# Kernel tuning notes

Measured on AMD Instinct MI355X. Metric: run time of the kernel, lower is better.

The kernel has to match this reference:

```python
import jax, jax.numpy as jnp
import numpy as np

N, E = 50000, 800000
F_IN, C_PRE, C, G_HID = 16, 32, 64, 64
EPS = 1e-5


def graph_norm(x, batch, w, b, ms):
    # PyG GraphNorm over a single graph (batch all zeros)
    cnt = jax.ops.segment_sum(jnp.ones((x.shape[0], 1), x.dtype), batch, num_segments=1)
    mean = jax.ops.segment_sum(x, batch, num_segments=1) / cnt
    out = x - mean[batch] * ms
    var = jax.ops.segment_sum(out * out, batch, num_segments=1) / cnt
    std = jnp.sqrt(var + EPS)
    return w * out / std[batch] + b


def ggnn_conv(h, edge_index, edge_attr,
              gw1, gb1, gw2, gb2, gw3, gb3,
              zw, zb, rw, rb, hw, hb):
    n = h.shape[0]
    loops = jnp.arange(n)
    row = jnp.concatenate([edge_index[0], loops])  # sources (x_j)
    col = jnp.concatenate([edge_index[1], loops])  # targets (x_i), aggregation index
    ea = jnp.concatenate([edge_attr, jnp.ones((n, 1), h.dtype)], axis=0)
    deg = jax.ops.segment_sum(jnp.ones(col.shape[0], h.dtype), col, num_segments=n)
    dis = jnp.where(deg > 0, deg ** -0.5, 0.0)
    norm = dis[row] * dis[col]
    x_j = h[row]
    x_i = h[col]
    g = jnp.concatenate([x_i, x_j, ea], axis=-1)            # [E+N, 2C+1]
    g = jax.nn.relu(g @ gw1 + gb1)
    g = jax.nn.relu(g @ gw2 + gb2)
    gate = jax.nn.sigmoid(g @ gw3 + gb3)                     # [E+N, 1]
    msg = gate * (norm[:, None] * x_j)
    aggr = jax.ops.segment_sum(msg, col, num_segments=n)     # scatter-add
    zi = jnp.concatenate([h, aggr], axis=-1)
    z = jax.nn.sigmoid(zi @ zw + zb)
    r = jax.nn.sigmoid(zi @ rw + rb)
    hc = jax.nn.relu(jnp.concatenate([r * h, aggr], axis=-1) @ hw + hb)
    return (1.0 - z) * h + z * hc


def setup_inputs() -> dict:
    key = jax.random.key(0)
    ks = iter(jax.random.split(key, 40))

    def lin(k, fi, fo):
        return jax.random.normal(k, (fi, fo), jnp.float32) / np.sqrt(fi)

    inp = {
        'x': jax.random.normal(next(ks), (N, F_IN), jnp.float32),
        'edge_index': jax.random.randint(next(ks), (2, E), 0, N),
        'edge_attr': jax.random.uniform(next(ks), (E, 1), jnp.float32),
        'batch': jnp.zeros((N,), jnp.int32),
        'preproc_w': lin(next(ks), F_IN, C_PRE), 'preproc_b': jnp.zeros((C_PRE,), jnp.float32),
        'gn_pre_w': jnp.ones((C_PRE,), jnp.float32), 'gn_pre_b': jnp.zeros((C_PRE,), jnp.float32), 'gn_pre_ms': jnp.ones((C_PRE,), jnp.float32),
        'init_w': lin(next(ks), C_PRE, C), 'init_b': jnp.zeros((C,), jnp.float32),
        'gn_init_w': jnp.ones((C,), jnp.float32), 'gn_init_b': jnp.zeros((C,), jnp.float32), 'gn_init_ms': jnp.ones((C,), jnp.float32),
        'gate_w1': lin(next(ks), 2 * C + 1, G_HID), 'gate_b1': jnp.zeros((G_HID,), jnp.float32),
        'gate_w2': lin(next(ks), G_HID, G_HID), 'gate_b2': jnp.zeros((G_HID,), jnp.float32),
        'gate_w3': lin(next(ks), G_HID, 1), 'gate_b3': jnp.zeros((1,), jnp.float32),
        'lin_z_w': lin(next(ks), 2 * C, C), 'lin_z_b': jnp.zeros((C,), jnp.float32),
        'lin_r_w': lin(next(ks), 2 * C, C), 'lin_r_b': jnp.zeros((C,), jnp.float32),
        'lin_h_w': lin(next(ks), 2 * C, C), 'lin_h_b': jnp.zeros((C,), jnp.float32),
        'gn_ggnn_w': jnp.ones((C,), jnp.float32), 'gn_ggnn_b': jnp.zeros((C,), jnp.float32), 'gn_ggnn_ms': jnp.ones((C,), jnp.float32),
        'fc1_w': lin(next(ks), 2 * C, C), 'fc1_b': jnp.zeros((C,), jnp.float32),
        'gn_fc1_w': jnp.ones((C,), jnp.float32), 'gn_fc1_b': jnp.zeros((C,), jnp.float32), 'gn_fc1_ms': jnp.ones((C,), jnp.float32),
        'fc2_w': lin(next(ks), C, 2), 'fc2_b': jnp.zeros((2,), jnp.float32),
    }
    return inp


def reference(x, edge_index, edge_attr, batch,
              preproc_w, preproc_b, gn_pre_w, gn_pre_b, gn_pre_ms,
              init_w, init_b, gn_init_w, gn_init_b, gn_init_ms,
              gate_w1, gate_b1, gate_w2, gate_b2, gate_w3, gate_b3,
              lin_z_w, lin_z_b, lin_r_w, lin_r_b, lin_h_w, lin_h_b,
              gn_ggnn_w, gn_ggnn_b, gn_ggnn_ms,
              fc1_w, fc1_b, gn_fc1_w, gn_fc1_b, gn_fc1_ms,
              fc2_w, fc2_b):
    n_layers = 4
    h = x @ preproc_w + preproc_b
    h = graph_norm(h, batch, gn_pre_w, gn_pre_b, gn_pre_ms)
    h = jax.nn.relu(h)
    h0 = h @ init_w + init_b
    h0 = graph_norm(h0, batch, gn_init_w, gn_init_b, gn_init_ms)
    h0 = jax.nn.relu(h0)
    h = h0
    for _ in range(n_layers):  # tied GGNN layer
        h = ggnn_conv(h, edge_index, edge_attr,
                      gate_w1, gate_b1, gate_w2, gate_b2, gate_w3, gate_b3,
                      lin_z_w, lin_z_b, lin_r_w, lin_r_b, lin_h_w, lin_h_b)
        h = graph_norm(h, batch, gn_ggnn_w, gn_ggnn_b, gn_ggnn_ms)
    out = jnp.concatenate([h0, h], axis=1)
    out = out @ fc1_w + fc1_b
    out = graph_norm(out, batch, gn_fc1_w, gn_fc1_b, gn_fc1_ms)
    out = jax.nn.relu(out)
    out = out @ fc2_w + fc2_b  # [N, 2] logits
    return out
```

## Files before the change

### kernel.cpp

```cpp
#include <hip/hip_runtime.h>

#define GN_EPS 1e-5f

typedef _Float16 half8 __attribute__((ext_vector_type(8)));
typedef float floatx4 __attribute__((ext_vector_type(4)));

__device__ __forceinline__ float sigmoidf_(float x){ return 1.0f/(1.0f+__expf(-x)); }
__device__ __forceinline__ float bcast_(float v, int k){
  return __int_as_float(__builtin_amdgcn_readlane(__float_as_int(v), k));
}

__global__ void cnt_init_kernel(int* cnt, int n){
  int i = blockIdx.x*blockDim.x+threadIdx.x;
  if (i < n) cnt[i] = 1;
}
__global__ void cnt_kernel(const int* __restrict__ ei, int* cnt, int E){
  int e = blockIdx.x*blockDim.x+threadIdx.x;
  if (e < E) atomicAdd(&cnt[ei[E+e]], 1);
}
__global__ void dis_from_cnt_kernel(const int* __restrict__ cnt, float* dis, int n){
  int i = blockIdx.x*blockDim.x+threadIdx.x;
  if (i < n) dis[i] = rsqrtf((float)cnt[i]);
}
__global__ __launch_bounds__(256) void scan1_kernel(const int* __restrict__ cnt,
                                                    int* loc, int* bsum, int n){
  __shared__ int s[256];
  int t = threadIdx.x, i = blockIdx.x*256 + t;
  int v = (i < n) ? cnt[i] : 0;
  s[t] = v; __syncthreads();
  #pragma unroll
  for (int d = 1; d < 256; d <<= 1){
    int u = (t >= d) ? s[t-d] : 0; __syncthreads();
    s[t] += u; __syncthreads();
  }
  if (i < n) loc[i] = s[t] - v;
  if (t == 255) bsum[blockIdx.x] = s[255];
}
__global__ __launch_bounds__(256) void scan2_kernel(int* bsum, int nb){
  __shared__ int s[256];
  int t = threadIdx.x;
  int v = (t < nb) ? bsum[t] : 0;
  s[t] = v; __syncthreads();
  #pragma unroll
  for (int d = 1; d < 256; d <<= 1){
    int u = (t >= d) ? s[t-d] : 0; __syncthreads();
    s[t] += u; __syncthreads();
  }
  if (t < nb) bsum[t] = s[t] - v;
}
__global__ void scan3_kernel(const int* __restrict__ loc, const int* __restrict__ bsum,
                             int* rowptr, int n, int total){
  int i = blockIdx.x*blockDim.x+threadIdx.x;
  if (i < n) rowptr[i] = loc[i] + bsum[i >> 8];
  if (i == 0) rowptr[n] = total;
}
__global__ void scatter_kernel(const int* __restrict__ ei, const float* __restrict__ ea,
                               const int* __restrict__ rowptr, int* fill,
                               unsigned* sd, _Float16* ea2, int E, int n){
  int idx = blockIdx.x*blockDim.x+threadIdx.x;
  int tot = E + n;
  if (idx >= tot) return;
  int r, c; float v;
  if (idx < E){ r = ei[idx]; c = ei[E+idx]; v = ea[idx]; }
  else        { r = c = idx - E; v = 1.0f; }
  int j = rowptr[c] + atomicAdd(&fill[c], 1);
  sd[j] = (unsigned)r | ((unsigned)c << 16);
  ea2[j] = (_Float16)v;
}

__global__ __launch_bounds__(256) void wprep_kernel(
    const float* __restrict__ w1, const float* __restrict__ zw,
    const float* __restrict__ rw, const float* __restrict__ hw,
    const float* __restrict__ fw, const float* __restrict__ w2,
    _Float16* __restrict__ wp){
  int idx = blockIdx.x*256 + threadIdx.x;
  if (idx < 8192){
    int t=idx>>10, kh=(idx>>9)&1, g=(idx>>7)&3, l=(idx>>3)&15, j=idx&7;
    int kg=(t>=4?64:0)+kh*32+g*8+j;
    wp[idx] = (_Float16)w1[kg*64 + (t&3)*16 + l];
  } else if (idx < 40960){
    int m=(idx-8192)>>13, k=(idx-8192)&8191;
    int t=(k>>11)&3, kh=(k>>9)&3, g=(k>>7)&3, l=(k>>3)&15, j=k&7;
    const float* W = (m==0)?zw:((m==1)?rw:((m==2)?hw:fw));
    wp[idx] = (_Float16)W[(kh*32+g*8+j)*64 + t*16 + l];
  } else if (idx < 45056){
    int k = idx-40960;
    int t=(k>>10)&3, kh=(k>>9)&1, g=(k>>7)&3, l=(k>>3)&15, j=k&7;
    wp[idx] = (_Float16)w2[(kh*32+g*8+j)*64 + t*16 + l];
  }
}

template<int K_IN, int C_OUT>
__global__ __launch_bounds__(256) void mm1_kernel(
    const float* __restrict__ x, const float* __restrict__ W,
    const float* __restrict__ b, float* __restrict__ y, int n){
  __shared__ float sW[K_IN*C_OUT];
  for (int i = threadIdx.x; i < K_IN*C_OUT; i += 256) sW[i] = W[i];
  __syncthreads();
  const int lane = threadIdx.x & 63;
  const int col  = (lane < C_OUT) ? lane : 0;
  const float bias = b[col];
  int wid = (blockIdx.x*256 + threadIdx.x) >> 6;
  int nw  = (gridDim.x*256) >> 6;
  for (int i = wid; i < n; i += nw){
    float xv = (lane < K_IN) ? x[(size_t)i*K_IN + lane] : 0.0f;
    float a0 = bias, a1 = 0.0f;
    #pragma unroll
    for (int k = 0; k < K_IN; k += 2){
      a0 += bcast_(xv, k  ) * sW[(k  )*C_OUT + col];
      a1 += bcast_(xv, k+1) * sW[(k+1)*C_OUT + col];
    }
    if (lane < C_OUT) y[(size_t)i*C_OUT + lane] = a0 + a1;
  }
}

template<int RELU, int WRITE_H0>
__global__ __launch_bounds__(256) void normpq_kernel(
    const float* __restrict__ hin, float* __restrict__ hout,
    float* __restrict__ h0out,
    const float* __restrict__ stats,
    const float* __restrict__ gw, const float* __restrict__ gb,
    const float* __restrict__ gms,
    const _Float16* __restrict__ w1p, const float* __restrict__ b1,
    _Float16* __restrict__ Ph, _Float16* __restrict__ QH, int n)
{
  __shared__ _Float16 sB[8192];
  __shared__ float sSO[128];
  for (int i = threadIdx.x; i < 1024; i += 256)
    ((half8*)sB)[i] = ((const half8*)w1p)[i];
  if (threadIdx.x < 64){
    int ch = threadIdx.x;
    float invN = 1.0f/(float)n;
    float mean = stats[ch]*invN;
    float mm = mean*gms[ch];
    float var = stats[64+ch]*invN - mm*(2.0f*mean - mm);
    float inv = rsqrtf(fmaxf(var,0.f)+GN_EPS);
    float sc = inv*gw[ch];
    sSO[ch] = sc;
    sSO[64+ch] = gb[ch] - mm*sc;
  }
  __syncthreads();
  const int lane = threadIdx.x & 63;
  const int g16 = lane>>4, l16 = lane&15;
  float scA[8], ofA[8], scB[8], ofB[8];
  #pragma unroll
  for (int j = 0; j < 8; ++j){
    scA[j]=sSO[g16*8+j];    ofA[j]=sSO[64+g16*8+j];
    scB[j]=sSO[32+g16*8+j]; ofB[j]=sSO[96+g16*8+j];
  }
  float b1f[4];
  #pragma unroll
  for (int t = 0; t < 4; ++t) b1f[t] = b1[t*16 + l16];

  int wid = (blockIdx.x*blockDim.x + threadIdx.x) >> 6;
  int nw  = (gridDim.x*blockDim.x) >> 6;
  int tiles = (n + 15) >> 4;
  for (int tile = wid; tile < tiles; tile += nw){
    int base = tile*16;
    int na = min(base + l16, n-1);
    const float* hp = hin + (size_t)na*64;
    float4 a0 = *(const float4*)(hp + g16*8);
    float4 a1 = *(const float4*)(hp + g16*8 + 4);
    float4 c0 = *(const float4*)(hp + 32 + g16*8);
    float4 c1 = *(const float4*)(hp + 32 + g16*8 + 4);
    float va[8] = {a0.x,a0.y,a0.z,a0.w,a1.x,a1.y,a1.z,a1.w};
    float vb[8] = {c0.x,c0.y,c0.z,c0.w,c1.x,c1.y,c1.z,c1.w};
    half8 af0, af1;
    #pragma unroll
    for (int j = 0; j < 8; ++j){
      float v = va[j]*scA[j] + ofA[j];
      if (RELU) v = fmaxf(v, 0.f);
      va[j] = v; af0[j] = (_Float16)v;
      float u = vb[j]*scB[j] + ofB[j];
      if (RELU) u = fmaxf(u, 0.f);
      vb[j] = u; af1[j] = (_Float16)u;
    }
    float* op = hout + (size_t)na*64;
    *(float4*)(op + g16*8)       = (float4){va[0],va[1],va[2],va[3]};
    *(float4*)(op + g16*8 + 4)   = (float4){va[4],va[5],va[6],va[7]};
    *(float4*)(op + 32 + g16*8)  = (float4){vb[0],vb[1],vb[2],vb[3]};
    *(float4*)(op + 32 + g16*8+4)= (float4){vb[4],vb[5],vb[6],vb[7]};
    if (WRITE_H0){
      float* o2 = h0out + (size_t)na*64;
      *(float4*)(o2 + g16*8)       = (float4){va[0],va[1],va[2],va[3]};
      *(float4*)(o2 + g16*8 + 4)   = (float4){va[4],va[5],va[6],va[7]};
      *(float4*)(o2 + 32 + g16*8)  = (float4){vb[0],vb[1],vb[2],vb[3]};
      *(float4*)(o2 + 32 + g16*8+4)= (float4){vb[4],vb[5],vb[6],vb[7]};
    }
    *(half8*)(QH + (size_t)na*128 + 64 + g16*8) = af0;
    *(half8*)(QH + (size_t)na*128 + 96 + g16*8) = af1;

    floatx4 acc[8];
    #pragma unroll
    for (int t = 0; t < 8; ++t){
      float bv = (t < 4) ? b1f[t] : 0.0f;
      acc[t] = (floatx4){bv, bv, bv, bv};
    }
    #pragma unroll
    for (int t = 0; t < 8; ++t){
      half8 bf0 = *(const half8*)&sB[((t*2+0)*4+g16)*128 + l16*8];
      half8 bf1 = *(const half8*)&sB[((t*2+1)*4+g16)*128 + l16*8];
      acc[t] = __builtin_amdgcn_mfma_f32_16x16x32_f16(af0, bf0, acc[t], 0, 0, 0);
      acc[t] = __builtin_amdgcn_mfma_f32_16x16x32_f16(af1, bf1, acc[t], 0, 0, 0);
    }
    #pragma unroll
    for (int t = 0; t < 8; ++t)
      #pragma unroll
      for (int rg = 0; rg < 4; ++rg){
        int nd = base + g16*4 + rg;
        if (nd < n){
          if (t < 4) Ph[(size_t)nd*64  + t*16 + l16]      = (_Float16)acc[t][rg];
          else       QH[(size_t)nd*128 + (t-4)*16 + l16]  = (_Float16)acc[t][rg];
        }
      }
  }
}

__global__ __launch_bounds__(256) void gru_mfma_kernel(
    float* __restrict__ h, float* __restrict__ aggr,
    const float* __restrict__ dis, const _Float16* __restrict__ QH,
    const _Float16* __restrict__ gwp,
    const float* __restrict__ zb, const float* __restrict__ rb,
    const float* __restrict__ hb,
    float* __restrict__ stats, int n)
{
  __shared__ _Float16 sW[3*8192];
  __shared__ _Float16 sRH[4][16][72];
  __shared__ float sSt[128];
  if (threadIdx.x < 128) sSt[threadIdx.x] = 0.f;
  for (int i = threadIdx.x; i < 3072; i += 256)
    ((half8*)sW)[i] = ((const half8*)gwp)[i];
  __syncthreads();
  const int lane = threadIdx.x & 63;
  const int g16 = lane>>4, l16 = lane&15;
  const int w = threadIdx.x >> 6;
  float zbf[4], rbf[4], hbf[4];
  #pragma unroll
  for (int t = 0; t < 4; ++t){
    zbf[t] = zb[t*16+l16]; rbf[t] = rb[t*16+l16]; hbf[t] = hb[t*16+l16];
  }
  float ssum[4] = {0,0,0,0}, ssq[4] = {0,0,0,0};
#define GW(m,t,kh) (*(const half8*)&sW[(m)*8192 + (((t)*4+(kh))*4+g16)*128 + l16*8])

  int wid = (blockIdx.x*blockDim.x + threadIdx.x) >> 6;
  int nw  = (gridDim.x*blockDim.x) >> 6;
  int tiles = (n + 15) >> 4;
  for (int tile = wid; tile < tiles; tile += nw){
    int base = tile*16;
    int na = min(base + l16, n-1);
    float dv = dis[na];
    half8 af[4];
    af[0] = *(const half8*)(QH + (size_t)na*128 + 64 + g16*8);
    af[1] = *(const half8*)(QH + (size_t)na*128 + 96 + g16*8);
    #pragma unroll
    for (int kh = 0; kh < 2; ++kh){
      float* ar = aggr + (size_t)na*64 + kh*32 + g16*8;
      float4 a0 = *(const float4*)ar;
      float4 a1 = *(const float4*)(ar+4);
      *(float4*)(ar)   = (float4){0,0,0,0};
      *(float4*)(ar+4) = (float4){0,0,0,0};
      half8 t8;
      t8[0]=(_Float16)(a0.x*dv); t8[1]=(_Float16)(a0.y*dv);
      t8[2]=(_Float16)(a0.z*dv); t8[3]=(_Float16)(a0.w*dv);
      t8[4]=(_Float16)(a1.x*dv); t8[5]=(_Float16)(a1.y*dv);
      t8[6]=(_Float16)(a1.z*dv); t8[7]=(_Float16)(a1.w*dv);
      af[2+kh] = t8;
    }
    floatx4 az[4], ar4[4];
    #pragma unroll
    for (int t = 0; t < 4; ++t){
      az[t]  = (floatx4){zbf[t], zbf[t], zbf[t], zbf[t]};
      ar4[t] = (floatx4){rbf[t], rbf[t], rbf[t], rbf[t]};
      #pragma unroll
      for (int kh = 0; kh < 4; ++kh){
        az[t]  = __builtin_amdgcn_mfma_f32_16x16x32_f16(af[kh], GW(0,t,kh), az[t],  0, 0, 0);
        ar4[t] = __builtin_amdgcn_mfma_f32_16x16x32_f16(af[kh], GW(1,t,kh), ar4[t], 0, 0, 0);
      }
    }
    float zr[16], hv[16];
    #pragma unroll
    for (int t = 0; t < 4; ++t)
      #pragma unroll
      for (int rg = 0; rg < 4; ++rg){
        int ndc = min(base + g16*4 + rg, n-1);
        float hval = h[(size_t)ndc*64 + t*16 + l16];
        float zv = sigmoidf_(az[t][rg]);
        float rv = sigmoidf_(ar4[t][rg]);
        zr[t*4+rg] = zv; hv[t*4+rg] = hval;
        sRH[w][g16*4+rg][t*16+l16] = (_Float16)(rv*hval);
      }
    asm volatile("s_waitcnt lgkmcnt(0)" ::: "memory");
    __builtin_amdgcn_sched_barrier(0);
    half8 af2_0 = *(const half8*)&sRH[w][l16][g16*8];
    half8 af2_1 = *(const half8*)&sRH[w][l16][32 + g16*8];
    floatx4 ah[4];
    #pragma unroll
    for (int t = 0; t < 4; ++t){
      ah[t] = (floatx4){hbf[t], hbf[t], hbf[t], hbf[t]};
      ah[t] = __builtin_amdgcn_mfma_f32_16x16x32_f16(af2_0, GW(2,t,0), ah[t], 0, 0, 0);
      ah[t] = __builtin_amdgcn_mfma_f32_16x16x32_f16(af2_1, GW(2,t,1), ah[t], 0, 0, 0);
      ah[t] = __builtin_amdgcn_mfma_f32_16x16x32_f16(af[2],  GW(2,t,2), ah[t], 0, 0, 0);
      ah[t] = __builtin_amdgcn_mfma_f32_16x16x32_f16(af[3],  GW(2,t,3), ah[t], 0, 0, 0);
    }
    #pragma unroll
    for (int t = 0; t < 4; ++t)
      #pragma unroll
      for (int rg = 0; rg < 4; ++rg){
        int nd = base + g16*4 + rg;
        if (nd < n){
          float hc = fmaxf(ah[t][rg], 0.f);
          float zv = zr[t*4+rg];
          float hn = (1.f - zv)*hv[t*4+rg] + zv*hc;
          h[(size_t)nd*64 + t*16 + l16] = hn;
          ssum[t] += hn; ssq[t] += hn*hn;
        }
      }
  }
#undef GW
  #pragma unroll
  for (int t = 0; t < 4; ++t){
    atomicAdd(&sSt[t*16+l16], ssum[t]);
    atomicAdd(&sSt[64+t*16+l16], ssq[t]);
  }
  __syncthreads();
  if (threadIdx.x < 128) atomicAdd(&stats[threadIdx.x], sSt[threadIdx.x]);
}

__global__ __launch_bounds__(256) void fc1_mfma_kernel(
    const float* __restrict__ h0, const float* __restrict__ h,
    const _Float16* __restrict__ fp, const float* __restrict__ b,
    float* __restrict__ out, float* __restrict__ stats, int n)
{
  __shared__ _Float16 sB[8192];
  __shared__ float sSt[128];
  if (threadIdx.x < 128) sSt[threadIdx.x] = 0.f;
  for (int i = threadIdx.x; i < 1024; i += 256)
    ((half8*)sB)[i] = ((const half8*)fp)[i];
  __syncthreads();
  const int lane = threadIdx.x & 63;
  const int g16 = lane>>4, l16 = lane&15;
  float bf[4];
  #pragma unroll
  for (int t = 0; t < 4; ++t) bf[t] = b[t*16+l16];
  float ssum[4] = {0,0,0,0}, ssq[4] = {0,0,0,0};

  int wid = (blockIdx.x*blockDim.x + threadIdx.x) >> 6;
  int nw  = (gridDim.x*blockDim.x) >> 6;
  int tiles = (n + 15) >> 4;
  for (int tile = wid; tile < tiles; tile += nw){
    int base = tile*16;
    int na = min(base + l16, n-1);
    half8 af[4];
    #pragma unroll
    for (int kh = 0; kh < 4; ++kh){
      const float* sp = (kh < 2 ? h0 : h) + (size_t)na*64 + (kh&1)*32 + g16*8;
      float4 a0 = *(const float4*)sp;
      float4 a1 = *(const float4*)(sp+4);
      half8 t8;
      t8[0]=(_Float16)a0.x; t8[1]=(_Float16)a0.y; t8[2]=(_Float16)a0.z; t8[3]=(_Float16)a0.w;
      t8[4]=(_Float16)a1.x; t8[5]=(_Float16)a1.y; t8[6]=(_Float16)a1.z; t8[7]=(_Float16)a1.w;
      af[kh] = t8;
    }
    #pragma unroll
    for (int t = 0; t < 4; ++t){
      floatx4 acc = (floatx4){bf[t], bf[t], bf[t], bf[t]};
      #pragma unroll
      for (int kh = 0; kh < 4; ++kh)
        acc = __builtin_amdgcn_mfma_f32_16x16x32_f16(af[kh],
                *(const half8*)&sB[((t*4+kh)*4+g16)*128 + l16*8], acc, 0, 0, 0);
      #pragma unroll
      for (int rg = 0; rg < 4; ++rg){
        int nd = base + g16*4 + rg;
        if (nd < n){
          float v = acc[rg];
          out[(size_t)nd*64 + t*16 + l16] = v;
          ssum[t] += v; ssq[t] += v*v;
        }
      }
    }
  }
  #pragma unroll
  for (int t = 0; t < 4; ++t){
    atomicAdd(&sSt[t*16+l16], ssum[t]);
    atomicAdd(&sSt[64+t*16+l16], ssq[t]);
  }
  __syncthreads();
  if (threadIdx.x < 128) atomicAdd(&stats[threadIdx.x], sSt[threadIdx.x]);
}

__global__ __launch_bounds__(256) void edge_tile_kernel(
    const unsigned* __restrict__ sd, const _Float16* __restrict__ ea2,
    const _Float16* __restrict__ Ph, const _Float16* __restrict__ QH,
    const float* __restrict__ dis,
    const _Float16* __restrict__ w2p, const float* __restrict__ b2,
    const float* __restrict__ w1e, const float* __restrict__ w3,
    const float* __restrict__ b3,
    float* __restrict__ aggr, float* __restrict__ stats, int EN)
{
  if (blockIdx.x == 0 && threadIdx.x < 128) stats[threadIdx.x] = 0.f;

  const int lane = threadIdx.x & 63;
  const int g16  = lane >> 4;
  const int l16  = lane & 15;

  half8 bfrag[4][2];
  #pragma unroll
  for (int t = 0; t < 4; ++t)
    #pragma unroll
    for (int kh = 0; kh < 2; ++kh)
      bfrag[t][kh] = *(const half8*)&w2p[t*1024 + kh*512 + g16*128 + l16*8];

  half8 w1h[2];
  #pragma unroll
  for (int kh = 0; kh < 2; ++kh)
    #pragma unroll
    for (int j = 0; j < 8; ++j)
      w1h[kh][j] = (_Float16)w1e[kh*32 + g16*8 + j];

  float w3f[4], b2f[4];
  #pragma unroll
  for (int t = 0; t < 4; ++t){ w3f[t] = w3[t*16 + l16]; b2f[t] = b2[t*16 + l16]; }
  const float b3v = b3[0];
  const _Float16* QHh = QH + 64;

  int wid = (blockIdx.x*blockDim.x + threadIdx.x) >> 6;
  int nw  = (gridDim.x*blockDim.x) >> 6;
  int tiles = (EN + 15) >> 4;

  for (int tile = wid; tile < tiles; tile += nw){
    int e0 = tile << 4;
    int m = EN - e0; if (m > 16) m = 16;
    int el = e0 + ((l16 < m) ? l16 : (m-1));
    unsigned sdv = sd[el];
    int r = (int)(sdv & 0xffffu);
    int c = (int)(sdv >> 16);
    float dv = (l16 < m) ? dis[r] : 0.0f;
    _Float16 eavh = ea2[el];

    half8 hq0 = *(const half8*)(QH + (size_t)r*128 + g16*8);
    half8 hq1 = *(const half8*)(QH + (size_t)r*128 + 32 + g16*8);
    half8 p0  = *(const half8*)(Ph + (size_t)c*64 + g16*8);
    half8 p1  = *(const half8*)(Ph + (size_t)c*64 + 32 + g16*8);

    _Float16 hv16[16];
    #pragma unroll
    for (int i = 0; i < 16; ++i){
      int ri = __builtin_amdgcn_readlane(r, i);
      hv16[i] = QHh[(size_t)ri*128 + lane];
    }

    half8 e8;
    #pragma unroll
    for (int j = 0; j < 8; ++j) e8[j] = eavh;
    half8 a0h = p0 + hq0 + w1h[0]*e8;
    half8 a1h = p1 + hq1 + w1h[1]*e8;
    #pragma unroll
    for (int j = 0; j < 8; ++j){
      a0h[j] = a0h[j] > (_Float16)0.f ? a0h[j] : (_Float16)0.f;
      a1h[j] = a1h[j] > (_Float16)0.f ? a1h[j] : (_Float16)0.f;
    }

    floatx4 acc[4];
    #pragma unroll
    for (int t4 = 0; t4 < 4; ++t4)
      acc[t4] = (floatx4){b2f[t4], b2f[t4], b2f[t4], b2f[t4]};
    __builtin_amdgcn_s_setprio(1);
    #pragma unroll
    for (int t4 = 0; t4 < 4; ++t4){
      acc[t4] = __builtin_amdgcn_mfma_f32_16x16x32_f16(a0h, bfrag[t4][0], acc[t4], 0, 0, 0);
      acc[t4] = __builtin_amdgcn_mfma_f32_16x16x32_f16(a1h, bfrag[t4][1], acc[t4], 0, 0, 0);
    }
    __builtin_amdgcn_s_setprio(0);

    float s[4] = {0.f,0.f,0.f,0.f};
    #pragma unroll
    for (int t4 = 0; t4 < 4; ++t4)
      #pragma unroll
      for (int rg = 0; rg < 4; ++rg)
        s[rg] += fmaxf(acc[t4][rg], 0.0f) * w3f[t4];
    #pragma unroll
    for (int rg = 0; rg < 4; ++rg){
      #pragma unroll
      for (int off = 1; off < 16; off <<= 1)
        s[rg] += __shfl_xor(s[rg], off);
      s[rg] = sigmoidf_(s[rg] + b3v);
    }

    float fs[4];
    #pragma unroll
    for (int rg = 0; rg < 4; ++rg){
      float dvp = __shfl(dv, (g16 << 4) | (g16*4 + rg));
      fs[rg] = s[rg] * dvp;
    }

    int cnext = __shfl(c, (lane & 48) | ((l16 + 1) & 15));
    unsigned long long bm = __ballot(c != cnext);
    unsigned bmask = ((unsigned)bm | 0x8000u) & 0xffffu;

    float accv = 0.f;
    #pragma unroll
    for (int i = 0; i < 16; ++i){
      float gi = bcast_(fs[i & 3], (i >> 2) << 4);
      accv = fmaf(gi, (float)hv16[i], accv);
      if ((bmask >> i) & 1){
        int ci = __builtin_amdgcn_readlane(c, i);
        atomicAdd(&aggr[(size_t)ci*64 + lane], accv);
        accv = 0.f;
      }
    }
  }
}

template<int C>
__global__ __launch_bounds__(256) void norm_stats_kernel(
    const float* __restrict__ x, int n, float* __restrict__ stats){
  __shared__ float ssum[256], ssq[256];
  const int tid = threadIdx.x;
  const int c = tid % C;
  int row = (blockIdx.x*256 + tid) / C;
  int stride = (gridDim.x*256) / C;
  float s = 0.f, q = 0.f;
  for (int i = row; i < n; i += stride){
    float v = x[(size_t)i*C + c];
    s += v; q += v*v;
  }
  ssum[tid] = s; ssq[tid] = q;
  __syncthreads();
  if (tid < C){
    float S = 0.f, Q2 = 0.f;
    for (int t = tid; t < 256; t += C){ S += ssum[t]; Q2 += ssq[t]; }
    atomicAdd(&stats[tid], S);
    atomicAdd(&stats[C + tid], Q2);
  }
}

template<int C, int RELU>
__global__ __launch_bounds__(256) void norm_apply_kernel(
    const float* __restrict__ x, const float* __restrict__ stats,
    const float* __restrict__ w, const float* __restrict__ b,
    const float* __restrict__ ms, float* __restrict__ y, int n){
  const float invN = 1.0f / (float)n;
  size_t idx = blockIdx.x*256 + threadIdx.x;
  size_t step = (size_t)gridDim.x*256;
  size_t tot = (size_t)n*C;
  for (; idx < tot; idx += step){
    int c = idx % C;
    float mean = stats[c] * invN;
    float mm = mean * ms[c];
    float var = stats[C + c]*invN - mm*(2.0f*mean - mm);
    float inv = rsqrtf(fmaxf(var, 0.0f) + GN_EPS);
    float v = (x[idx] - mm)*inv*w[c] + b[c];
    if (RELU) v = fmaxf(v, 0.0f);
    y[idx] = v;
  }
}

__global__ void fc2_kernel(
    const float* __restrict__ x, const float* __restrict__ w,
    const float* __restrict__ b, float* __restrict__ out, int n){
  int i = blockIdx.x*blockDim.x + threadIdx.x;
  if (i >= n) return;
  float a0 = b[0], a1 = b[1];
  const float4* xr = (const float4*)(x + (size_t)i*64);
  #pragma unroll
  for (int k4 = 0; k4 < 16; ++k4){
    float4 v = xr[k4];
    int k = k4*4;
    a0 += v.x*w[(k+0)*2+0] + v.y*w[(k+1)*2+0] + v.z*w[(k+2)*2+0] + v.w*w[(k+3)*2+0];
    a1 += v.x*w[(k+0)*2+1] + v.y*w[(k+1)*2+1] + v.z*w[(k+2)*2+1] + v.w*w[(k+3)*2+1];
  }
  out[i*2+0] = a0;
  out[i*2+1] = a1;
}

extern "C" void kernel_launch(void* const* d_in, const int* in_sizes, int n_in,
                              void* d_out, int out_size, void* d_ws, size_t ws_size,
                              hipStream_t stream){
  const float* x          = (const float*)d_in[0];
  const int*   ei         = (const int*)  d_in[1];
  const float* ea         = (const float*)d_in[2];
  const float* preproc_w  = (const float*)d_in[4];
  const float* preproc_b  = (const float*)d_in[5];
  const float* gn_pre_w   = (const float*)d_in[6];
  const float* gn_pre_b   = (const float*)d_in[7];
  const float* gn_pre_ms  = (const float*)d_in[8];
  const float* init_w     = (const float*)d_in[9];
  const float* init_b     = (const float*)d_in[10];
  const float* gn_init_w  = (const float*)d_in[11];
  const float* gn_init_b  = (const float*)d_in[12];
  const float* gn_init_ms = (const float*)d_in[13];
  const float* gate_w1    = (const float*)d_in[14];
  const float* gate_b1    = (const float*)d_in[15];
  const float* gate_w2    = (const float*)d_in[16];
  const float* gate_b2    = (const float*)d_in[17];
  const float* gate_w3    = (const float*)d_in[18];
  const float* gate_b3    = (const float*)d_in[19];
  const float* lin_z_w    = (const float*)d_in[20];
  const float* lin_z_b    = (const float*)d_in[21];
  const float* lin_r_w    = (const float*)d_in[22];
  const float* lin_r_b    = (const float*)d_in[23];
  const float* lin_h_w    = (const float*)d_in[24];
  const float* lin_h_b    = (const float*)d_in[25];
  const float* gn_ggnn_w  = (const float*)d_in[26];
  const float* gn_ggnn_b  = (const float*)d_in[27];
  const float* gn_ggnn_ms = (const float*)d_in[28];
  const float* fc1_w      = (const float*)d_in[29];
  const float* fc1_b      = (const float*)d_in[30];
  const float* gn_fc1_w   = (const float*)d_in[31];
  const float* gn_fc1_b   = (const float*)d_in[32];
  const float* gn_fc1_ms  = (const float*)d_in[33];
  const float* fc2_w      = (const float*)d_in[34];
  const float* fc2_b      = (const float*)d_in[35];

  const int N = in_sizes[3];
  const int E = in_sizes[1] / 2;
  const int EN = E + N;

  float* base = (float*)d_ws;
  const size_t R = (size_t)64*N;
  float* h     = base;
  float* h0    = h    + R;
  float* Preg  = h0   + R;
  float* aggr  = Preg + R;
  float* QHreg = aggr + R;
  float* dis   = QHreg + R;
  float* stats = dis + N;
  size_t need = (5*R + N + 128) * sizeof(float);
  if (ws_size < need || N > 65535) return;

  _Float16* Ph  = (_Float16*)Preg;
  _Float16* QH  = (_Float16*)QHreg;
  unsigned* sd  = (unsigned*)(Preg + 32*(size_t)N);
  _Float16* ea2 = (_Float16*)(sd + EN);
  _Float16* wp  = (_Float16*)(((uintptr_t)(ea2 + EN) + 15) & ~(uintptr_t)15);
  _Float16* w1p = wp;
  _Float16* gwp = wp + 8192;
  _Float16* fc1p= wp + 32768;
  _Float16* w2p = wp + 40960;

  int* cnt    = (int*)aggr;
  int* loc    = cnt + N;
  int* fill   = loc + N;
  int* bsum   = fill + N;
  int* rowptr = bsum + 256;

  const int GB = 1024;
  const int RB = 784;
  const int EB = 3072;
  const int nb = (N + 255) / 256;

  cnt_init_kernel<<<(N+255)/256, 256, 0, stream>>>(cnt, N);
  cnt_kernel<<<(E+255)/256, 256, 0, stream>>>(ei, cnt, E);
  dis_from_cnt_kernel<<<(N+255)/256, 256, 0, stream>>>(cnt, dis, N);
  scan1_kernel<<<nb, 256, 0, stream>>>(cnt, loc, bsum, N);
  scan2_kernel<<<1, 256, 0, stream>>>(bsum, nb);
  scan3_kernel<<<nb, 256, 0, stream>>>(loc, bsum, rowptr, N, EN);
  hipMemsetAsync(fill, 0, (size_t)N*sizeof(int), stream);
  scatter_kernel<<<(EN+255)/256, 256, 0, stream>>>(ei, ea, rowptr, fill, sd, ea2, E, N);
  wprep_kernel<<<176, 256, 0, stream>>>(gate_w1, lin_z_w, lin_r_w, lin_h_w, fc1_w, gate_w2, wp);
  hipMemsetAsync(aggr, 0, R*sizeof(float), stream);

  mm1_kernel<16,32><<<GB, 256, 0, stream>>>(x, preproc_w, preproc_b, h0, N);
  hipMemsetAsync(stats, 0, 2*64*sizeof(float), stream);
  norm_stats_kernel<32><<<256, 256, 0, stream>>>(h0, N, stats);
  norm_apply_kernel<32,1><<<2048, 256, 0, stream>>>(h0, stats, gn_pre_w, gn_pre_b, gn_pre_ms, h, N);

  mm1_kernel<32,64><<<GB, 256, 0, stream>>>(h, init_w, init_b, h0, N);
  hipMemsetAsync(stats, 0, 2*64*sizeof(float), stream);
  norm_stats_kernel<64><<<256, 256, 0, stream>>>(h0, N, stats);
  normpq_kernel<1,1><<<RB, 256, 0, stream>>>(h0, h, h0, stats,
                                             gn_init_w, gn_init_b, gn_init_ms,
                                             w1p, gate_b1, Ph, QH, N);

  for (int layer = 0; layer < 4; ++layer){
    edge_tile_kernel<<<EB, 256, 0, stream>>>(sd, ea2, Ph, QH, dis,
                                             w2p, gate_b2, gate_w1 + 128*64,
                                             gate_w3, gate_b3, aggr, stats, EN);
    gru_mfma_kernel<<<RB, 256, 0, stream>>>(h, aggr, dis, QH, gwp,
                                            lin_z_b, lin_r_b, lin_h_b, stats, N);
    if (layer < 3)
      normpq_kernel<0,0><<<RB, 256, 0, stream>>>(h, h, nullptr, stats,
                                                 gn_ggnn_w, gn_ggnn_b, gn_ggnn_ms,
                                                 w1p, gate_b1, Ph, QH, N);
    else
      norm_apply_kernel<64,0><<<2048, 256, 0, stream>>>(h, stats, gn_ggnn_w, gn_ggnn_b, gn_ggnn_ms, h, N);
  }

  hipMemsetAsync(stats, 0, 2*64*sizeof(float), stream);
  fc1_mfma_kernel<<<RB, 256, 0, stream>>>(h0, h, fc1p, fc1_b, aggr, stats, N);
  norm_apply_kernel<64,1><<<2048, 256, 0, stream>>>(aggr, stats, gn_fc1_w, gn_fc1_b, gn_fc1_ms, h, N);

  fc2_kernel<<<(N+255)/256, 256, 0, stream>>>(h, fc2_w, fc2_b, (float*)d_out, N);
}
```

Measured before the change: 631.5 us.

## Software-pipeline edge tile gathers and fuse norm stats into mm1

The edge kernel is restructured into a two-stage software pipeline. Indices for tile t+2 are loaded and gathers for tile t+1 are issued while tile t is computed, so the latency of the random gathers is hidden behind MFMA work. The edge grid shrinks from 3072 to 2048 blocks, since each wave now holds two tiles' worth of registers. Separately, the graph-norm statistics are accumulated inside mm1_kernel, which removes two norm_stats launches and the re-read of h0. The cost is higher register pressure, which may lower occupancy.

```diff
diff --git a/kernel.cpp b/kernel.cpp
--- a/kernel.cpp
+++ b/kernel.cpp
@@ -90,11 +90,14 @@
   }
 }
 
-template<int K_IN, int C_OUT>
+template<int K_IN, int C_OUT, int STATS>
 __global__ __launch_bounds__(256) void mm1_kernel(
     const float* __restrict__ x, const float* __restrict__ W,
-    const float* __restrict__ b, float* __restrict__ y, int n){
+    const float* __restrict__ b, float* __restrict__ y,
+    float* __restrict__ stats, int n){
   __shared__ float sW[K_IN*C_OUT];
+  __shared__ float sSt[2*C_OUT];
+  if (STATS && threadIdx.x < 2*C_OUT) sSt[threadIdx.x] = 0.f;
   for (int i = threadIdx.x; i < K_IN*C_OUT; i += 256) sW[i] = W[i];
   __syncthreads();
   const int lane = threadIdx.x & 63;
@@ -102,6 +105,7 @@
   const float bias = b[col];
   int wid = (blockIdx.x*256 + threadIdx.x) >> 6;
   int nw  = (gridDim.x*256) >> 6;
+  float qs = 0.f, qq = 0.f;
   for (int i = wid; i < n; i += nw){
     float xv = (lane < K_IN) ? x[(size_t)i*K_IN + lane] : 0.0f;
     float a0 = bias, a1 = 0.0f;
@@ -110,7 +114,19 @@
       a0 += bcast_(xv, k  ) * sW[(k  )*C_OUT + col];
       a1 += bcast_(xv, k+1) * sW[(k+1)*C_OUT + col];
     }
-    if (lane < C_OUT) y[(size_t)i*C_OUT + lane] = a0 + a1;
+    if (lane < C_OUT){
+      float v = a0 + a1;
+      y[(size_t)i*C_OUT + lane] = v;
+      if (STATS){ qs += v; qq += v*v; }
+    }
+  }
+  if (STATS){
+    if (lane < C_OUT){
+      atomicAdd(&sSt[lane], qs);
+      atomicAdd(&sSt[C_OUT+lane], qq);
+    }
+    __syncthreads();
+    if (threadIdx.x < 2*C_OUT) atomicAdd(&stats[threadIdx.x], sSt[threadIdx.x]);
   }
 }
 
@@ -388,6 +404,82 @@
   if (threadIdx.x < 128) atomicAdd(&stats[threadIdx.x], sSt[threadIdx.x]);
 }
 
+#define EDGE_LOADSD(TT, SDV, EAV) do { \
+    int e0_ = (TT) << 4; int m_ = EN - e0_; if (m_ > 16) m_ = 16; \
+    int el_ = e0_ + ((l16 < m_) ? l16 : (m_ - 1)); \
+    SDV = sd[el_]; EAV = ea2[el_]; \
+  } while(0)
+
+#define EDGE_GATHER(G, TT, SDV, EAV) do { \
+    int e0_ = (TT) << 4; int m_ = EN - e0_; if (m_ > 16) m_ = 16; \
+    int r_ = (int)((SDV) & 0xffffu); \
+    G##_c  = (int)((SDV) >> 16); \
+    G##_ea = (EAV); \
+    G##_dv = (l16 < m_) ? dis[r_] : 0.0f; \
+    G##_hq0 = *(const half8*)(QH + (size_t)r_*128 + g16*8); \
+    G##_hq1 = *(const half8*)(QH + (size_t)r_*128 + 32 + g16*8); \
+    G##_p0  = *(const half8*)(Ph + (size_t)G##_c*64 + g16*8); \
+    G##_p1  = *(const half8*)(Ph + (size_t)G##_c*64 + 32 + g16*8); \
+    _Pragma("unroll") \
+    for (int i_ = 0; i_ < 8; ++i_){ \
+      int ri_ = __builtin_amdgcn_readlane(r_, i_); \
+      G##_hva[i_] = QHh[(size_t)ri_*128 + lane]; \
+    } \
+    _Pragma("unroll") \
+    for (int i_ = 0; i_ < 8; ++i_){ \
+      int ri_ = __builtin_amdgcn_readlane(r_, 8+i_); \
+      G##_hvb[i_] = QHh[(size_t)ri_*128 + lane]; \
+    } \
+  } while(0)
+
+#define EDGE_COMPUTE(G) do { \
+    half8 e8_; \
+    _Pragma("unroll") for (int j_ = 0; j_ < 8; ++j_) e8_[j_] = G##_ea; \
+    half8 a0_ = G##_p0 + G##_hq0 + w1h[0]*e8_; \
+    half8 a1_ = G##_p1 + G##_hq1 + w1h[1]*e8_; \
+    _Pragma("unroll") for (int j_ = 0; j_ < 8; ++j_){ \
+      a0_[j_] = a0_[j_] > (_Float16)0.f ? a0_[j_] : (_Float16)0.f; \
+      a1_[j_] = a1_[j_] > (_Float16)0.f ? a1_[j_] : (_Float16)0.f; \
+    } \
+    floatx4 acc_[4]; \
+    _Pragma("unroll") for (int t4_ = 0; t4_ < 4; ++t4_) \
+      acc_[t4_] = (floatx4){b2f[t4_], b2f[t4_], b2f[t4_], b2f[t4_]}; \
+    __builtin_amdgcn_s_setprio(1); \
+    _Pragma("unroll") for (int t4_ = 0; t4_ < 4; ++t4_){ \
+      acc_[t4_] = __builtin_amdgcn_mfma_f32_16x16x32_f16(a0_, bfrag[t4_][0], acc_[t4_], 0, 0, 0); \
+      acc_[t4_] = __builtin_amdgcn_mfma_f32_16x16x32_f16(a1_, bfrag[t4_][1], acc_[t4_], 0, 0, 0); \
+    } \
+    __builtin_amdgcn_s_setprio(0); \
+    float s_[4] = {0.f,0.f,0.f,0.f}; \
+    _Pragma("unroll") for (int t4_ = 0; t4_ < 4; ++t4_) \
+      _Pragma("unroll") for (int rg_ = 0; rg_ < 4; ++rg_) \
+        s_[rg_] += fmaxf(acc_[t4_][rg_], 0.0f) * w3f[t4_]; \
+    _Pragma("unroll") for (int rg_ = 0; rg_ < 4; ++rg_){ \
+      _Pragma("unroll") for (int off_ = 1; off_ < 16; off_ <<= 1) \
+        s_[rg_] += __shfl_xor(s_[rg_], off_); \
+      s_[rg_] = sigmoidf_(s_[rg_] + b3v); \
+    } \
+    float fs_[4]; \
+    _Pragma("unroll") for (int rg_ = 0; rg_ < 4; ++rg_){ \
+      float dvp_ = __shfl(G##_dv, (g16 << 4) | (g16*4 + rg_)); \
+      fs_[rg_] = s_[rg_] * dvp_; \
+    } \
+    int cnext_ = __shfl(G##_c, (lane & 48) | ((l16 + 1) & 15)); \
+    unsigned long long bm_ = __ballot(G##_c != cnext_); \
+    unsigned bmask_ = ((unsigned)bm_ | 0x8000u) & 0xffffu; \
+    float accv_ = 0.f; \
+    _Pragma("unroll") for (int i_ = 0; i_ < 16; ++i_){ \
+      float gi_ = bcast_(fs_[i_ & 3], (i_ >> 2) << 4); \
+      _Float16 hv_ = (i_ < 8) ? G##_hva[i_ & 7] : G##_hvb[i_ & 7]; \
+      accv_ = fmaf(gi_, (float)hv_, accv_); \
+      if ((bmask_ >> i_) & 1){ \
+        int ci_ = __builtin_amdgcn_readlane(G##_c, i_); \
+        atomicAdd(&aggr[(size_t)ci_*64 + lane], accv_); \
+        accv_ = 0.f; \
+      } \
+    } \
+  } while(0)
+
 __global__ __launch_bounds__(256) void edge_tile_kernel(
     const unsigned* __restrict__ sd, const _Float16* __restrict__ ea2,
     const _Float16* __restrict__ Ph, const _Float16* __restrict__ QH,
@@ -427,110 +519,36 @@
   int nw  = (gridDim.x*blockDim.x) >> 6;
   int tiles = (EN + 15) >> 4;
 
-  for (int tile = wid; tile < tiles; tile += nw){
-    int e0 = tile << 4;
-    int m = EN - e0; if (m > 16) m = 16;
-    int el = e0 + ((l16 < m) ? l16 : (m-1));
-    unsigned sdv = sd[el];
-    int r = (int)(sdv & 0xffffu);
-    int c = (int)(sdv >> 16);
-    float dv = (l16 < m) ? dis[r] : 0.0f;
-    _Float16 eavh = ea2[el];
-
-    half8 hq0 = *(const half8*)(QH + (size_t)r*128 + g16*8);
-    half8 hq1 = *(const half8*)(QH + (size_t)r*128 + 32 + g16*8);
-    half8 p0  = *(const half8*)(Ph + (size_t)c*64 + g16*8);
-    half8 p1  = *(const half8*)(Ph + (size_t)c*64 + 32 + g16*8);
-
-    _Float16 hv16[16];
-    #pragma unroll
-    for (int i = 0; i < 16; ++i){
-      int ri = __builtin_amdgcn_readlane(r, i);
-      hv16[i] = QHh[(size_t)ri*128 + lane];
-    }
-
-    half8 e8;
-    #pragma unroll
-    for (int j = 0; j < 8; ++j) e8[j] = eavh;
-    half8 a0h = p0 + hq0 + w1h[0]*e8;
-    half8 a1h = p1 + hq1 + w1h[1]*e8;
-    #pragma unroll
-    for (int j = 0; j < 8; ++j){
-      a0h[j] = a0h[j] > (_Float16)0.f ? a0h[j] : (_Float16)0.f;
-      a1h[j] = a1h[j] > (_Float16)0.f ? a1h[j] : (_Float16)0.f;
-    }
-
-    floatx4 acc[4];
-    #pragma unroll
-    for (int t4 = 0; t4 < 4; ++t4)
-      acc[t4] = (floatx4){b2f[t4], b2f[t4], b2f[t4], b2f[t4]};
-    __builtin_amdgcn_s_setprio(1);
-    #pragma unroll
-    for (int t4 = 0; t4 < 4; ++t4){
-      acc[t4] = __builtin_amdgcn_mfma_f32_16x16x32_f16(a0h, bfrag[t4][0], acc[t4], 0, 0, 0);
-      acc[t4] = __builtin_amdgcn_mfma_f32_16x16x32_f16(a1h, bfrag[t4][1], acc[t4], 0, 0, 0);
-    }
-    __builtin_amdgcn_s_setprio(0);
-
-    float s[4] = {0.f,0.f,0.f,0.f};
-    #pragma unroll
-    for (int t4 = 0; t4 < 4; ++t4)
-      #pragma unroll
-      for (int rg = 0; rg < 4; ++rg)
-        s[rg] += fmaxf(acc[t4][rg], 0.0f) * w3f[t4];
-    #pragma unroll
-    for (int rg = 0; rg < 4; ++rg){
-      #pragma unroll
-      for (int off = 1; off < 16; off <<= 1)
-        s[rg] += __shfl_xor(s[rg], off);
-      s[rg] = sigmoidf_(s[rg] + b3v);
-    }
-
-    float fs[4];
-    #pragma unroll
-    for (int rg = 0; rg < 4; ++rg){
-      float dvp = __shfl(dv, (g16 << 4) | (g16*4 + rg));
-      fs[rg] = s[rg] * dvp;
-    }
-
-    int cnext = __shfl(c, (lane & 48) | ((l16 + 1) & 15));
-    unsigned long long bm = __ballot(c != cnext);
-    unsigned bmask = ((unsigned)bm | 0x8000u) & 0xffffu;
-
-    float accv = 0.f;
-    #pragma unroll
-    for (int i = 0; i < 16; ++i){
-      float gi = bcast_(fs[i & 3], (i >> 2) << 4);
-      accv = fmaf(gi, (float)hv16[i], accv);
-      if ((bmask >> i) & 1){
-        int ci = __builtin_amdgcn_readlane(c, i);
-        atomicAdd(&aggr[(size_t)ci*64 + lane], accv);
-        accv = 0.f;
-      }
-    }
-  }
-}
-
-template<int C>
-__global__ __launch_bounds__(256) void norm_stats_kernel(
-    const float* __restrict__ x, int n, float* __restrict__ stats){
-  __shared__ float ssum[256], ssq[256];
-  const int tid = threadIdx.x;
-  const int c = tid % C;
-  int row = (blockIdx.x*256 + tid) / C;
-  int stride = (gridDim.x*256) / C;
-  float s = 0.f, q = 0.f;
-  for (int i = row; i < n; i += stride){
-    float v = x[(size_t)i*C + c];
-    s += v; q += v*v;
-  }
-  ssum[tid] = s; ssq[tid] = q;
-  __syncthreads();
-  if (tid < C){
-    float S = 0.f, Q2 = 0.f;
-    for (int t = tid; t < 256; t += C){ S += ssum[t]; Q2 += ssq[t]; }
-    atomicAdd(&stats[tid], S);
-    atomicAdd(&stats[C + tid], Q2);
+  int t0 = wid;
+  if (t0 >= tiles) return;
+
+  int A_c, B_c; float A_dv, B_dv; _Float16 A_ea, B_ea;
+  half8 A_hq0, A_hq1, A_p0, A_p1, A_hva, A_hvb;
+  half8 B_hq0, B_hq1, B_p0, B_p1, B_hva, B_hvb;
+  unsigned sd0, sd1; _Float16 ea0, ea1;
+
+  EDGE_LOADSD(t0, sd0, ea0);
+  int t1 = t0 + nw;
+  bool has1 = t1 < tiles;
+  if (has1) EDGE_LOADSD(t1, sd1, ea1);
+  EDGE_GATHER(A, t0, sd0, ea0);
+
+  for (;;){
+    int t2 = has1 ? t1 + nw : tiles;
+    bool has2 = t2 < tiles;
+    if (has2) EDGE_LOADSD(t2, sd0, ea0);
+    if (has1) EDGE_GATHER(B, t1, sd1, ea1);
+    EDGE_COMPUTE(A);
+    if (!has1) break;
+
+    int t3 = has2 ? t2 + nw : tiles;
+    bool has3 = t3 < tiles;
+    if (has3) EDGE_LOADSD(t3, sd1, ea1);
+    if (has2) EDGE_GATHER(A, t2, sd0, ea0);
+    EDGE_COMPUTE(B);
+    if (!has2) break;
+
+    t1 = t3; has1 = has3;
   }
 }
 
@@ -646,7 +664,7 @@
 
   const int GB = 1024;
   const int RB = 784;
-  const int EB = 3072;
+  const int EB = 2048;
   const int nb = (N + 255) / 256;
 
   cnt_init_kernel<<<(N+255)/256, 256, 0, stream>>>(cnt, N);
@@ -660,14 +678,12 @@
   wprep_kernel<<<176, 256, 0, stream>>>(gate_w1, lin_z_w, lin_r_w, lin_h_w, fc1_w, gate_w2, wp);
   hipMemsetAsync(aggr, 0, R*sizeof(float), stream);
 
-  mm1_kernel<16,32><<<GB, 256, 0, stream>>>(x, preproc_w, preproc_b, h0, N);
   hipMemsetAsync(stats, 0, 2*64*sizeof(float), stream);
-  norm_stats_kernel<32><<<256, 256, 0, stream>>>(h0, N, stats);
+  mm1_kernel<16,32,1><<<GB, 256, 0, stream>>>(x, preproc_w, preproc_b, h0, stats, N);
   norm_apply_kernel<32,1><<<2048, 256, 0, stream>>>(h0, stats, gn_pre_w, gn_pre_b, gn_pre_ms, h, N);
 
-  mm1_kernel<32,64><<<GB, 256, 0, stream>>>(h, init_w, init_b, h0, N);
   hipMemsetAsync(stats, 0, 2*64*sizeof(float), stream);
-  norm_stats_kernel<64><<<256, 256, 0, stream>>>(h0, N, stats);
+  mm1_kernel<32,64,1><<<GB, 256, 0, stream>>>(h, init_w, init_b, h0, stats, N);
   normpq_kernel<1,1><<<RB, 256, 0, stream>>>(h0, h, h0, stats,
                                              gn_init_w, gn_init_b, gn_init_ms,
                                              w1p, gate_b1, Ph, QH, N);
```

After: 693.3 us. +9.8%, slower.
